# Performance work log

Measured on AMD Instinct MI355X. Metric: run time of the kernel, lower is better.

The kernel has to match this reference:

```python
import jax, jax.numpy as jnp
import numpy as np

K = 9  # kernel_size (knn neighbors, loop=True -> self included)

def setup_inputs() -> dict:
    key = jax.random.key(0)
    k1, k2, k3 = jax.random.split(key, 3)
    B, C, H, W = 8, 64, 32, 32
    OUT = 64
    x = jax.random.normal(k1, (B, C, H, W), dtype=jnp.float32)
    # SAGEConv params: lin_l (neighbor aggregate, with bias), lin_r (root, no bias)
    s = 1.0 / np.sqrt(C)
    W_l = jax.random.uniform(k2, (OUT, C), minval=-s, maxval=s, dtype=jnp.float32)
    b_l = jnp.zeros((OUT,), dtype=jnp.float32)
    W_r = jax.random.uniform(k3, (OUT, C), minval=-s, maxval=s, dtype=jnp.float32)
    return {"x": x, "W_l": W_l, "b_l": b_l, "W_r": W_r}

def _knn_mean(x_f, batches):
    # squared-euclidean pairwise distances [N, N], masked across batches
    sq = jnp.sum(x_f * x_f, axis=-1)
    dist = sq[:, None] + sq[None, :] - 2.0 * (x_f @ x_f.T)
    cross = batches[:, None] != batches[None, :]
    dist = jnp.where(cross, jnp.inf, dist)
    neg, idx = jax.lax.top_k(-dist, K)          # k nearest (self included, dist 0)
    valid = (neg != -jnp.inf).astype(x_f.dtype)  # handle degenerate last-batch node
    nbr = x_f[idx] * valid[..., None]            # [N, K, C]
    return nbr.sum(axis=1) / valid.sum(axis=1, keepdims=True)

def reference(x, W_l, b_l, W_r):
    B, C, H, Wd = x.shape
    N = B * H * Wd
    x_f = x.transpose(0, 2, 3, 1).reshape(N, C)  # flat_nodes: [B*H*W, C]
    # torch.linspace(0, B, steps=N).to(int64): truncation of i*B/(N-1)
    batches = jnp.linspace(0.0, float(B), N).astype(jnp.int32)
    mean_nbr = _knn_mean(x_f, batches)
    # SAGEConv: lin_l(mean_j x_j) + lin_r(x_i)
    return mean_nbr @ W_l.T + b_l + x_f @ W_r.T
```

## Files before the change

### kernel.cpp

```cpp
#include <hip/hip_runtime.h>
#include <cstdint>
#include <cstddef>


__global__ __launch_bounds__(256, 2) void k_dist(const float* __restrict__ x,
                                                 float* __restrict__ xf,
                                                 float* __restrict__ D) {
  __shared__ float4 As4[32 * 33];
  __shared__ float4 Bs4[32 * 33];
  __shared__ float sqA[128];
  __shared__ float sqB[128];
  int cx = blockIdx.x;
  int i0 = (int)blockIdx.y << 7;
  int s = (i0 >= 7168) ? 7168 : (i0 & ~1023);
  int j0 = s + (cx << 7);
  const float* xA = x + (((size_t)(i0 >> 10)) << 16) + (i0 & 1023);
  const float* xB = x + (((size_t)(j0 >> 10)) << 16) + (j0 & 1023);
  int t = threadIdx.x;
  int tx = t & 15, ty = t >> 4;

  float acc[8][8];
#pragma unroll
  for (int r = 0; r < 8; ++r)
#pragma unroll
    for (int c = 0; c < 8; ++c) acc[r][c] = 0.f;

#pragma unroll 1
  for (int pass = 0; pass < 2; ++pass) {
    if (pass) __syncthreads();
    int c0 = pass << 5;
#pragma unroll
    for (int i = 0; i < 4; ++i) {
      int u = t + (i << 8);
      int c = u >> 5, m4 = u & 31;
      As4[c * 33 + m4] = *(const float4*)&xA[((size_t)(c0 + c) << 10) + (m4 << 2)];
      Bs4[c * 33 + m4] = *(const float4*)&xB[((size_t)(c0 + c) << 10) + (m4 << 2)];
    }
    __syncthreads();
    {
      int m = t & 127;
      const float* base = (t < 128) ? (const float*)As4 : (const float*)Bs4;
      float p = 0.f;
#pragma unroll
      for (int c = 0; c < 32; ++c) {
        float v = base[(c * 33 + (m >> 2)) * 4 + (m & 3)];
        p = fmaf(v, v, p);
      }
      float* dst = (t < 128) ? sqA : sqB;
      if (pass == 0) dst[m] = p; else dst[m] += p;
    }
    if (cx == 0) {
#pragma unroll
      for (int i = 0; i < 16; ++i) {
        int u = t + (i << 8);
        int c = u & 31, m = u >> 5;
        xf[((size_t)(i0 + m) << 6) + c0 + c] =
            ((const float*)As4)[(c * 33 + (m >> 2)) * 4 + (m & 3)];
      }
    }
#pragma unroll 4
    for (int k = 0; k < 32; ++k) {
      float4 a0 = As4[k * 33 + ty];
      float4 a1 = As4[k * 33 + 16 + ty];
      float4 b0 = Bs4[k * 33 + tx];
      float4 b1 = Bs4[k * 33 + 16 + tx];
      float av[8] = {a0.x, a0.y, a0.z, a0.w, a1.x, a1.y, a1.z, a1.w};
      float bv[8] = {b0.x, b0.y, b0.z, b0.w, b1.x, b1.y, b1.z, b1.w};
#pragma unroll
      for (int r = 0; r < 8; ++r)
#pragma unroll
        for (int c = 0; c < 8; ++c)
          acc[r][c] = fmaf(av[r], bv[c], acc[r][c]);
    }
  }
  __syncthreads();

  int rloc[8], cloc[8];
#pragma unroll
  for (int r = 0; r < 4; ++r) { rloc[r] = (ty << 2) + r; rloc[4 + r] = 64 + (ty << 2) + r; }
#pragma unroll
  for (int c = 0; c < 4; ++c) { cloc[c] = (tx << 2) + c; cloc[4 + c] = 64 + (tx << 2) + c; }
  float sqi[8], sqj[8];
#pragma unroll
  for (int r = 0; r < 8; ++r) sqi[r] = sqA[rloc[r]];
#pragma unroll
  for (int c = 0; c < 8; ++c) sqj[c] = sqB[cloc[c]];
#pragma unroll
  for (int r = 0; r < 8; ++r) {
    size_t rb = ((size_t)(i0 + rloc[r]) << 10) + (cx << 7);
    float4 o0, o1;
    o0.x = sqi[r] + sqj[0] - 2.f * acc[r][0];
    o0.y = sqi[r] + sqj[1] - 2.f * acc[r][1];
    o0.z = sqi[r] + sqj[2] - 2.f * acc[r][2];
    o0.w = sqi[r] + sqj[3] - 2.f * acc[r][3];
    o1.x = sqi[r] + sqj[4] - 2.f * acc[r][4];
    o1.y = sqi[r] + sqj[5] - 2.f * acc[r][5];
    o1.z = sqi[r] + sqj[6] - 2.f * acc[r][6];
    o1.w = sqi[r] + sqj[7] - 2.f * acc[r][7];
    *(float4*)&D[rb + (tx << 2)] = o0;
    *(float4*)&D[rb + 64 + (tx << 2)] = o1;
  }
}

__global__ __launch_bounds__(256, 2) void k_selout(const float* __restrict__ D,
                                                   const float* __restrict__ xf,
                                                   const float* __restrict__ Wl,
                                                   const float* __restrict__ bl,
                                                   const float* __restrict__ Wr,
                                                   float* __restrict__ out) {
  __shared__ float WsL[64][65];
  __shared__ float WsR[64][65];
  int t = threadIdx.x;
#pragma unroll
  for (int i = 0; i < 16; ++i) {
    int lin = t + (i << 8);
    WsL[lin >> 6][lin & 63] = Wl[lin];
    WsR[lin >> 6][lin & 63] = Wr[lin];
  }
  __syncthreads();
  int lane = t & 63;
  float wl[64], wr[64];
#pragma unroll
  for (int c = 0; c < 64; ++c) { wl[c] = WsL[lane][c]; wr[c] = WsR[lane][c]; }
  float bias = bl[lane];
  int w = t >> 6;
  int n0 = ((int)blockIdx.x << 4) + (w << 2);

  unsigned j9[4][9];
#pragma unroll
  for (int r = 0; r < 4; ++r) {
    int n = n0 + r;
    if (n == 8191) { j9[r][0] = 8191u; continue; }
    int s = (n >= 7168) ? 7168 : (n & ~1023);
    bool mlast = (n >= 7168);
    const float* drow = D + ((size_t)n << 10);
    unsigned long long cand[16];
#pragma unroll
    for (int q = 0; q < 4; ++q) {
      float4 v = *(const float4*)&drow[(lane << 4) + (q << 2)];
      float vv[4] = {v.x, v.y, v.z, v.w};
#pragma unroll
      for (int e = 0; e < 4; ++e) {
        int slot = (q << 2) + e;
        unsigned u = __float_as_uint(vv[e]);
        u = (u & 0x80000000u) ? ~u : (u | 0x80000000u);
        cand[slot] = ((unsigned long long)u << 32) | (unsigned)((lane << 4) + slot);
      }
    }
    if (mlast && lane == 63) cand[15] = ~0ull;
    unsigned long long m1 = cand[0], m2 = cand[1];
    if (m2 < m1) { unsigned long long tt = m1; m1 = m2; m2 = tt; }
#pragma unroll
    for (int q = 2; q < 16; ++q) {
      unsigned long long c = cand[q];
      unsigned long long lo = (c < m1) ? c : m1;
      unsigned long long hi = (c < m1) ? m1 : c;
      m2 = (hi < m2) ? hi : m2;
      m1 = lo;
    }
    unsigned long long lm = m1;
    unsigned rmask = 0;
    bool stale = false;
#pragma unroll
    for (int kk = 0; kk < 9; ++kk) {
      unsigned long long g = lm;
#pragma unroll
      for (int off = 32; off; off >>= 1) {
        unsigned ghi = __shfl_xor((unsigned)(g >> 32), off, 64);
        unsigned glo = __shfl_xor((unsigned)g, off, 64);
        unsigned long long o = ((unsigned long long)ghi << 32) | glo;
        g = (o < g) ? o : g;
      }
      j9[r][kk] = (unsigned)s + ((unsigned)g & 1023u);
      if (lm == g) {
        rmask |= 1u << (unsigned)(g & 15u);
        if (!stale) { lm = m2; stale = true; }
        else {
          unsigned long long best = ~0ull;
#pragma unroll
          for (int q = 0; q < 16; ++q) {
            bool alive = ((rmask >> q) & 1u) == 0u;
            unsigned long long c = cand[q];
            best = (alive && c < best) ? c : best;
          }
          lm = best;
        }
      }
    }
  }

  float ms[4], xr[4];
#pragma unroll
  for (int r = 0; r < 4; ++r) {
    int n = n0 + r;
    int cnt = (n == 8191) ? 1 : 9;
    float msum = 0.f;
    for (int k = 0; k < cnt; ++k)
      msum += xf[((size_t)j9[r][k] << 6) + lane];
    ms[r] = msum / (float)cnt;
    xr[r] = xf[((size_t)n << 6) + lane];
  }
  float accL[4] = {0.f, 0.f, 0.f, 0.f};
  float accR[4] = {0.f, 0.f, 0.f, 0.f};
#pragma unroll
  for (int c = 0; c < 64; ++c) {
#pragma unroll
    for (int r = 0; r < 4; ++r) {
      float mc = __int_as_float(__builtin_amdgcn_readlane(__float_as_int(ms[r]), c));
      float xc = __int_as_float(__builtin_amdgcn_readlane(__float_as_int(xr[r]), c));
      accL[r] = fmaf(mc, wl[c], accL[r]);
      accR[r] = fmaf(xc, wr[c], accR[r]);
    }
  }
#pragma unroll
  for (int r = 0; r < 4; ++r)
    out[((size_t)(n0 + r) << 6) + lane] = accL[r] + accR[r] + bias;
}

extern "C" void kernel_launch(void* const* d_in, const int* in_sizes, int n_in,
                              void* d_out, int out_size, void* d_ws, size_t ws_size,
                              hipStream_t stream) {
  const float* x  = (const float*)d_in[0];
  const float* Wl = (const float*)d_in[1];
  const float* bl = (const float*)d_in[2];
  const float* Wr = (const float*)d_in[3];
  float* out = (float*)d_out;

  char* ws = (char*)d_ws;
  float* xf = (float*)(ws);
  float* D  = (float*)(ws + 2097152);

  k_dist<<<dim3(8, 64), 256, 0, stream>>>(x, xf, D);
  k_selout<<<512, 256, 0, stream>>>(D, xf, Wl, bl, Wr, out);
}
```

Measured before the change: 106.5 us.

## Apply linear layers before neighbor gather and fold projection into distance kernel

Because the mean commutes with the linear map, x·W_l^T and x·W_r^T (plus bias) are now computed once per node as extra GEMM tiles inside the distance kernel, using 64 extra blocks that reuse the tiled FMA path. The selection kernel then averages nine projected rows instead of running a per-row 64x64 matvec held in registers, which frees registers and lets it use one wave per node with higher occupancy. The load of distance candidates is also reordered so each wave reads contiguously (lane-strided float4). The xf transpose buffer is dropped; the cost is extra workspace for the yl/yr buffers and a small rounding difference from reordering the sum.

```diff
diff --git a/kernel.cpp b/kernel.cpp
--- a/kernel.cpp
+++ b/kernel.cpp
@@ -4,18 +4,28 @@
 
 
 __global__ __launch_bounds__(256, 2) void k_dist(const float* __restrict__ x,
-                                                 float* __restrict__ xf,
+                                                 const float* __restrict__ Wl,
+                                                 const float* __restrict__ Wr,
+                                                 const float* __restrict__ bl,
+                                                 float* __restrict__ yl,
+                                                 float* __restrict__ yr,
                                                  float* __restrict__ D) {
   __shared__ float4 As4[32 * 33];
   __shared__ float4 Bs4[32 * 33];
   __shared__ float sqA[128];
   __shared__ float sqB[128];
-  int cx = blockIdx.x;
-  int i0 = (int)blockIdx.y << 7;
-  int s = (i0 >= 7168) ? 7168 : (i0 & ~1023);
-  int j0 = s + (cx << 7);
+  int bx = blockIdx.x, by = blockIdx.y;
+  bool is_w = (by >= 64);
+  int i0, j0 = 0;
+  if (is_w) {
+    i0 = (((by - 64) << 3) + bx) << 7;
+  } else {
+    i0 = by << 7;
+    int s = (i0 >= 7168) ? 7168 : (i0 & ~1023);
+    j0 = s + (bx << 7);
+  }
   const float* xA = x + (((size_t)(i0 >> 10)) << 16) + (i0 & 1023);
-  const float* xB = x + (((size_t)(j0 >> 10)) << 16) + (j0 & 1023);
+  const float* xB = is_w ? xA : x + (((size_t)(j0 >> 10)) << 16) + (j0 & 1023);
   int t = threadIdx.x;
   int tx = t & 15, ty = t >> 4;
 
@@ -34,10 +44,26 @@
       int u = t + (i << 8);
       int c = u >> 5, m4 = u & 31;
       As4[c * 33 + m4] = *(const float4*)&xA[((size_t)(c0 + c) << 10) + (m4 << 2)];
-      Bs4[c * 33 + m4] = *(const float4*)&xB[((size_t)(c0 + c) << 10) + (m4 << 2)];
+    }
+    if (!is_w) {
+#pragma unroll
+      for (int i = 0; i < 4; ++i) {
+        int u = t + (i << 8);
+        int c = u >> 5, m4 = u & 31;
+        Bs4[c * 33 + m4] = *(const float4*)&xB[((size_t)(c0 + c) << 10) + (m4 << 2)];
+      }
+    } else {
+#pragma unroll
+      for (int i = 0; i < 16; ++i) {
+        int u = t + (i << 8);
+        int j = u >> 5, c = u & 31;
+        const float* Wsrc = (j < 64) ? Wl : Wr;
+        int jr = j & 63;
+        ((float*)&Bs4[c * 33 + (j >> 2)])[j & 3] = Wsrc[(jr << 6) + c0 + c];
+      }
     }
     __syncthreads();
-    {
+    if (!is_w) {
       int m = t & 127;
       const float* base = (t < 128) ? (const float*)As4 : (const float*)Bs4;
       float p = 0.f;
@@ -48,15 +74,6 @@
       }
       float* dst = (t < 128) ? sqA : sqB;
       if (pass == 0) dst[m] = p; else dst[m] += p;
-    }
-    if (cx == 0) {
-#pragma unroll
-      for (int i = 0; i < 16; ++i) {
-        int u = t + (i << 8);
-        int c = u & 31, m = u >> 5;
-        xf[((size_t)(i0 + m) << 6) + c0 + c] =
-            ((const float*)As4)[(c * 33 + (m >> 2)) * 4 + (m & 3)];
-      }
     }
 #pragma unroll 4
     for (int k = 0; k < 32; ++k) {
@@ -75,9 +92,26 @@
   }
   __syncthreads();
 
-  int rloc[8], cloc[8];
+  int rloc[8];
 #pragma unroll
   for (int r = 0; r < 4; ++r) { rloc[r] = (ty << 2) + r; rloc[4 + r] = 64 + (ty << 2) + r; }
+
+  if (is_w) {
+    float4 blv = *(const float4*)&bl[tx << 2];
+#pragma unroll
+    for (int r = 0; r < 8; ++r) {
+      int n = i0 + rloc[r];
+      float4 o0, o1;
+      o0.x = acc[r][0]; o0.y = acc[r][1]; o0.z = acc[r][2]; o0.w = acc[r][3];
+      o1.x = acc[r][4] + blv.x; o1.y = acc[r][5] + blv.y;
+      o1.z = acc[r][6] + blv.z; o1.w = acc[r][7] + blv.w;
+      *(float4*)&yl[((size_t)n << 6) + (tx << 2)] = o0;
+      *(float4*)&yr[((size_t)n << 6) + (tx << 2)] = o1;
+    }
+    return;
+  }
+
+  int cloc[8];
 #pragma unroll
   for (int c = 0; c < 4; ++c) { cloc[c] = (tx << 2) + c; cloc[4 + c] = 64 + (tx << 2) + c; }
   float sqi[8], sqj[8];
@@ -87,7 +121,7 @@
   for (int c = 0; c < 8; ++c) sqj[c] = sqB[cloc[c]];
 #pragma unroll
   for (int r = 0; r < 8; ++r) {
-    size_t rb = ((size_t)(i0 + rloc[r]) << 10) + (cx << 7);
+    size_t rb = ((size_t)(i0 + rloc[r]) << 10) + (bx << 7);
     float4 o0, o1;
     o0.x = sqi[r] + sqj[0] - 2.f * acc[r][0];
     o0.y = sqi[r] + sqj[1] - 2.f * acc[r][1];
@@ -102,49 +136,34 @@
   }
 }
 
-__global__ __launch_bounds__(256, 2) void k_selout(const float* __restrict__ D,
-                                                   const float* __restrict__ xf,
-                                                   const float* __restrict__ Wl,
-                                                   const float* __restrict__ bl,
-                                                   const float* __restrict__ Wr,
+__global__ __launch_bounds__(256, 4) void k_selout(const float* __restrict__ D,
+                                                   const float* __restrict__ yl,
+                                                   const float* __restrict__ yr,
                                                    float* __restrict__ out) {
-  __shared__ float WsL[64][65];
-  __shared__ float WsR[64][65];
   int t = threadIdx.x;
-#pragma unroll
-  for (int i = 0; i < 16; ++i) {
-    int lin = t + (i << 8);
-    WsL[lin >> 6][lin & 63] = Wl[lin];
-    WsR[lin >> 6][lin & 63] = Wr[lin];
-  }
-  __syncthreads();
   int lane = t & 63;
-  float wl[64], wr[64];
-#pragma unroll
-  for (int c = 0; c < 64; ++c) { wl[c] = WsL[lane][c]; wr[c] = WsR[lane][c]; }
-  float bias = bl[lane];
   int w = t >> 6;
-  int n0 = ((int)blockIdx.x << 4) + (w << 2);
-
-  unsigned j9[4][9];
-#pragma unroll
-  for (int r = 0; r < 4; ++r) {
-    int n = n0 + r;
-    if (n == 8191) { j9[r][0] = 8191u; continue; }
+  int n = ((int)blockIdx.x << 2) + w;
+
+  float rv = yr[((size_t)n << 6) + lane];
+  float acc;
+  if (n == 8191) {
+    acc = yl[((size_t)n << 6) + lane];
+  } else {
     int s = (n >= 7168) ? 7168 : (n & ~1023);
     bool mlast = (n >= 7168);
     const float* drow = D + ((size_t)n << 10);
     unsigned long long cand[16];
 #pragma unroll
     for (int q = 0; q < 4; ++q) {
-      float4 v = *(const float4*)&drow[(lane << 4) + (q << 2)];
+      float4 v = *(const float4*)&drow[(q << 8) + (lane << 2)];
       float vv[4] = {v.x, v.y, v.z, v.w};
 #pragma unroll
       for (int e = 0; e < 4; ++e) {
-        int slot = (q << 2) + e;
         unsigned u = __float_as_uint(vv[e]);
         u = (u & 0x80000000u) ? ~u : (u | 0x80000000u);
-        cand[slot] = ((unsigned long long)u << 32) | (unsigned)((lane << 4) + slot);
+        unsigned jj = (unsigned)((q << 8) + (lane << 2) + e);
+        cand[(q << 2) + e] = ((unsigned long long)u << 32) | jj;
       }
     }
     if (mlast && lane == 63) cand[15] = ~0ull;
@@ -161,6 +180,7 @@
     unsigned long long lm = m1;
     unsigned rmask = 0;
     bool stale = false;
+    unsigned j9[9];
 #pragma unroll
     for (int kk = 0; kk < 9; ++kk) {
       unsigned long long g = lm;
@@ -171,9 +191,10 @@
         unsigned long long o = ((unsigned long long)ghi << 32) | glo;
         g = (o < g) ? o : g;
       }
-      j9[r][kk] = (unsigned)s + ((unsigned)g & 1023u);
+      j9[kk] = (unsigned)s + ((unsigned)g & 1023u);
       if (lm == g) {
-        rmask |= 1u << (unsigned)(g & 15u);
+        unsigned slot = (((unsigned)g >> 6) & 12u) | ((unsigned)g & 3u);
+        rmask |= 1u << slot;
         if (!stale) { lm = m2; stale = true; }
         else {
           unsigned long long best = ~0ull;
@@ -187,34 +208,18 @@
         }
       }
     }
-  }
-
-  float ms[4], xr[4];
-#pragma unroll
-  for (int r = 0; r < 4; ++r) {
-    int n = n0 + r;
-    int cnt = (n == 8191) ? 1 : 9;
-    float msum = 0.f;
-    for (int k = 0; k < cnt; ++k)
-      msum += xf[((size_t)j9[r][k] << 6) + lane];
-    ms[r] = msum / (float)cnt;
-    xr[r] = xf[((size_t)n << 6) + lane];
-  }
-  float accL[4] = {0.f, 0.f, 0.f, 0.f};
-  float accR[4] = {0.f, 0.f, 0.f, 0.f};
-#pragma unroll
-  for (int c = 0; c < 64; ++c) {
-#pragma unroll
-    for (int r = 0; r < 4; ++r) {
-      float mc = __int_as_float(__builtin_amdgcn_readlane(__float_as_int(ms[r]), c));
-      float xc = __int_as_float(__builtin_amdgcn_readlane(__float_as_int(xr[r]), c));
-      accL[r] = fmaf(mc, wl[c], accL[r]);
-      accR[r] = fmaf(xc, wr[c], accR[r]);
-    }
-  }
-#pragma unroll
-  for (int r = 0; r < 4; ++r)
-    out[((size_t)(n0 + r) << 6) + lane] = accL[r] + accR[r] + bias;
+    float g0 = yl[((size_t)j9[0] << 6) + lane];
+    float g1 = yl[((size_t)j9[1] << 6) + lane];
+    float g2 = yl[((size_t)j9[2] << 6) + lane];
+    float g3 = yl[((size_t)j9[3] << 6) + lane];
+    float g4 = yl[((size_t)j9[4] << 6) + lane];
+    float g5 = yl[((size_t)j9[5] << 6) + lane];
+    float g6 = yl[((size_t)j9[6] << 6) + lane];
+    float g7 = yl[((size_t)j9[7] << 6) + lane];
+    float g8 = yl[((size_t)j9[8] << 6) + lane];
+    acc = (((g0 + g1) + (g2 + g3)) + ((g4 + g5) + (g6 + g7)) + g8) * (1.f / 9.f);
+  }
+  out[((size_t)n << 6) + lane] = acc + rv;
 }
 
 extern "C" void kernel_launch(void* const* d_in, const int* in_sizes, int n_in,
@@ -227,9 +232,10 @@
   float* out = (float*)d_out;
 
   char* ws = (char*)d_ws;
-  float* xf = (float*)(ws);
-  float* D  = (float*)(ws + 2097152);
-
-  k_dist<<<dim3(8, 64), 256, 0, stream>>>(x, xf, D);
-  k_selout<<<512, 256, 0, stream>>>(D, xf, Wl, bl, Wr, out);
+  float* yl = (float*)(ws);
+  float* yr = (float*)(ws + 2097152);
+  float* D  = (float*)(ws + 4194304);
+
+  k_dist<<<dim3(8, 72), 256, 0, stream>>>(x, Wl, Wr, bl, yl, yr, D);
+  k_selout<<<2048, 256, 0, stream>>>(D, yl, yr, out);
 }
```

After: 113.0 us. +6.2%, slower.

## Fuse distance, top-k selection and SAGE projection into one kernel via LDS

Applied to the files above, without the earlier changes.

Merges the distance kernel and the selection/output kernel into a single kernel. Each block computes a 16x1024 distance strip for its rows directly into shared memory, so the 8192x1024 distance matrix is never written to or read back from global memory. Neighbours are gathered straight from the original NCHW input, and the weights are staged in LDS instead of registers. In exchange, each block reloads its batch's full 1024-node feature slab and recomputes squared norms redundantly. It also uses about 72KB of LDS per block, which may limit occupancy.

```diff
diff --git a/kernel.cpp b/kernel.cpp
--- a/kernel.cpp
+++ b/kernel.cpp
@@ -3,67 +3,65 @@
 #include <cstddef>
 
 
-__global__ __launch_bounds__(256, 2) void k_dist(const float* __restrict__ x,
-                                                 float* __restrict__ xf,
-                                                 float* __restrict__ D) {
-  __shared__ float4 As4[32 * 33];
-  __shared__ float4 Bs4[32 * 33];
-  __shared__ float sqA[128];
-  __shared__ float sqB[128];
-  int cx = blockIdx.x;
-  int i0 = (int)blockIdx.y << 7;
-  int s = (i0 >= 7168) ? 7168 : (i0 & ~1023);
-  int j0 = s + (cx << 7);
-  const float* xA = x + (((size_t)(i0 >> 10)) << 16) + (i0 & 1023);
-  const float* xB = x + (((size_t)(j0 >> 10)) << 16) + (j0 & 1023);
-  int t = threadIdx.x;
-  int tx = t & 15, ty = t >> 4;
+typedef float nf4 __attribute__((ext_vector_type(4)));
+
+__global__ __launch_bounds__(256, 2) void k_all(const float* __restrict__ x,
+                                                const float* __restrict__ Wl,
+                                                const float* __restrict__ bl,
+                                                const float* __restrict__ Wr,
+                                                float* __restrict__ out) {
+  __shared__ float R0[16384];
+  __shared__ float Asf[1024];
+  __shared__ float sqX[1024];
+  float4* Xs4 = (float4*)R0;
+  float4* As4 = (float4*)Asf;
+  float4* sqX4 = (float4*)sqX;
+
+  int bi = (int)blockIdx.x, t = threadIdx.x;
+  int n0 = bi << 4;
+  int s = (n0 >= 7168) ? 7168 : (n0 & ~1023);
+  const float* xb = x + (((size_t)(s >> 10)) << 16);
+  const float* xrow = x + (((size_t)(n0 >> 10)) << 16) + (n0 & 1023);
+
+  {
+    int c = t >> 2, r4 = t & 3;
+    As4[(c << 2) + r4] = *(const float4*)&xrow[((size_t)c << 10) + (r4 << 2)];
+  }
 
   float acc[8][8];
 #pragma unroll
   for (int r = 0; r < 8; ++r)
 #pragma unroll
     for (int c = 0; c < 8; ++c) acc[r][c] = 0.f;
+  float4 p4 = {0.f, 0.f, 0.f, 0.f};
+  int h = t >> 7, cg = t & 127;
 
 #pragma unroll 1
-  for (int pass = 0; pass < 2; ++pass) {
-    if (pass) __syncthreads();
-    int c0 = pass << 5;
-#pragma unroll
-    for (int i = 0; i < 4; ++i) {
-      int u = t + (i << 8);
-      int c = u >> 5, m4 = u & 31;
-      As4[c * 33 + m4] = *(const float4*)&xA[((size_t)(c0 + c) << 10) + (m4 << 2)];
-      Bs4[c * 33 + m4] = *(const float4*)&xB[((size_t)(c0 + c) << 10) + (m4 << 2)];
+  for (int ks = 0; ks < 4; ++ks) {
+    if (ks) __syncthreads();
+    int k0 = ks << 4;
+#pragma unroll 4
+    for (int i = 0; i < 16; ++i) {
+      int lin = t + (i << 8);
+      int kc = lin >> 8, j4 = lin & 255;
+      Xs4[(kc << 8) + j4] =
+          *(const float4*)&xb[((size_t)(k0 + kc) << 10) + (j4 << 2)];
     }
     __syncthreads();
-    {
-      int m = t & 127;
-      const float* base = (t < 128) ? (const float*)As4 : (const float*)Bs4;
-      float p = 0.f;
-#pragma unroll
-      for (int c = 0; c < 32; ++c) {
-        float v = base[(c * 33 + (m >> 2)) * 4 + (m & 3)];
-        p = fmaf(v, v, p);
-      }
-      float* dst = (t < 128) ? sqA : sqB;
-      if (pass == 0) dst[m] = p; else dst[m] += p;
-    }
-    if (cx == 0) {
-#pragma unroll
-      for (int i = 0; i < 16; ++i) {
-        int u = t + (i << 8);
-        int c = u & 31, m = u >> 5;
-        xf[((size_t)(i0 + m) << 6) + c0 + c] =
-            ((const float*)As4)[(c * 33 + (m >> 2)) * 4 + (m & 3)];
-      }
-    }
-#pragma unroll 4
-    for (int k = 0; k < 32; ++k) {
-      float4 a0 = As4[k * 33 + ty];
-      float4 a1 = As4[k * 33 + 16 + ty];
-      float4 b0 = Bs4[k * 33 + tx];
-      float4 b1 = Bs4[k * 33 + 16 + tx];
+#pragma unroll
+    for (int kc = 0; kc < 16; ++kc) {
+      float4 v = Xs4[(kc << 8) + t];
+      p4.x = fmaf(v.x, v.x, p4.x);
+      p4.y = fmaf(v.y, v.y, p4.y);
+      p4.z = fmaf(v.z, v.z, p4.z);
+      p4.w = fmaf(v.w, v.w, p4.w);
+    }
+#pragma unroll
+    for (int kc = 0; kc < 16; ++kc) {
+      float4 a0 = As4[((k0 + kc) << 2) + (h << 1)];
+      float4 a1 = As4[((k0 + kc) << 2) + (h << 1) + 1];
+      float4 b0 = Xs4[(kc << 8) + cg];
+      float4 b1 = Xs4[(kc << 8) + 128 + cg];
       float av[8] = {a0.x, a0.y, a0.z, a0.w, a1.x, a1.y, a1.z, a1.w};
       float bv[8] = {b0.x, b0.y, b0.z, b0.w, b1.x, b1.y, b1.z, b1.w};
 #pragma unroll
@@ -73,78 +71,50 @@
           acc[r][c] = fmaf(av[r], bv[c], acc[r][c]);
     }
   }
-  __syncthreads();
-
-  int rloc[8], cloc[8];
-#pragma unroll
-  for (int r = 0; r < 4; ++r) { rloc[r] = (ty << 2) + r; rloc[4 + r] = 64 + (ty << 2) + r; }
-#pragma unroll
-  for (int c = 0; c < 4; ++c) { cloc[c] = (tx << 2) + c; cloc[4 + c] = 64 + (tx << 2) + c; }
-  float sqi[8], sqj[8];
-#pragma unroll
-  for (int r = 0; r < 8; ++r) sqi[r] = sqA[rloc[r]];
-#pragma unroll
-  for (int c = 0; c < 8; ++c) sqj[c] = sqB[cloc[c]];
-#pragma unroll
-  for (int r = 0; r < 8; ++r) {
-    size_t rb = ((size_t)(i0 + rloc[r]) << 10) + (cx << 7);
-    float4 o0, o1;
-    o0.x = sqi[r] + sqj[0] - 2.f * acc[r][0];
-    o0.y = sqi[r] + sqj[1] - 2.f * acc[r][1];
-    o0.z = sqi[r] + sqj[2] - 2.f * acc[r][2];
-    o0.w = sqi[r] + sqj[3] - 2.f * acc[r][3];
-    o1.x = sqi[r] + sqj[4] - 2.f * acc[r][4];
-    o1.y = sqi[r] + sqj[5] - 2.f * acc[r][5];
-    o1.z = sqi[r] + sqj[6] - 2.f * acc[r][6];
-    o1.w = sqi[r] + sqj[7] - 2.f * acc[r][7];
-    *(float4*)&D[rb + (tx << 2)] = o0;
-    *(float4*)&D[rb + 64 + (tx << 2)] = o1;
-  }
-}
-
-__global__ __launch_bounds__(256, 2) void k_selout(const float* __restrict__ D,
-                                                   const float* __restrict__ xf,
-                                                   const float* __restrict__ Wl,
-                                                   const float* __restrict__ bl,
-                                                   const float* __restrict__ Wr,
-                                                   float* __restrict__ out) {
-  __shared__ float WsL[64][65];
-  __shared__ float WsR[64][65];
-  int t = threadIdx.x;
-#pragma unroll
-  for (int i = 0; i < 16; ++i) {
-    int lin = t + (i << 8);
-    WsL[lin >> 6][lin & 63] = Wl[lin];
-    WsR[lin >> 6][lin & 63] = Wr[lin];
-  }
-  __syncthreads();
-  int lane = t & 63;
-  float wl[64], wr[64];
-#pragma unroll
-  for (int c = 0; c < 64; ++c) { wl[c] = WsL[lane][c]; wr[c] = WsR[lane][c]; }
-  float bias = bl[lane];
-  int w = t >> 6;
-  int n0 = ((int)blockIdx.x << 4) + (w << 2);
-
-  unsigned j9[4][9];
-#pragma unroll
-  for (int r = 0; r < 4; ++r) {
-    int n = n0 + r;
-    if (n == 8191) { j9[r][0] = 8191u; continue; }
-    int s = (n >= 7168) ? 7168 : (n & ~1023);
+  sqX4[t] = p4;
+  __syncthreads();
+
+  {
+    float4 sj0 = sqX4[cg];
+    float4 sj1 = sqX4[128 + cg];
+    int jb = (n0 - s) + (h << 3);
+#pragma unroll
+    for (int r = 0; r < 8; ++r) {
+      float si = sqX[jb + r];
+      nf4 o0 = {si + sj0.x - 2.f * acc[r][0], si + sj0.y - 2.f * acc[r][1],
+                si + sj0.z - 2.f * acc[r][2], si + sj0.w - 2.f * acc[r][3]};
+      nf4 o1 = {si + sj1.x - 2.f * acc[r][4], si + sj1.y - 2.f * acc[r][5],
+                si + sj1.z - 2.f * acc[r][6], si + sj1.w - 2.f * acc[r][7]};
+      int row = (h << 3) + r;
+      *(nf4*)&R0[(row << 10) + (cg << 2)] = o0;
+      *(nf4*)&R0[(row << 10) + 512 + (cg << 2)] = o1;
+    }
+  }
+  __syncthreads();
+
+  int lane = t & 63, w = t >> 6;
+  float msum[4], xr[4];
+  int cnt[4];
+#pragma unroll 1
+  for (int rr = 0; rr < 4; ++rr) {
+    int rl = (w << 2) + rr;
+    int n = n0 + rl;
+    float xself = x[(((size_t)(n >> 10)) << 16) + ((size_t)lane << 10) + (n & 1023)];
+    xr[rr] = xself;
+    if (n == 8191) { msum[rr] = xself; cnt[rr] = 1; continue; }
+    cnt[rr] = 9;
     bool mlast = (n >= 7168);
-    const float* drow = D + ((size_t)n << 10);
     unsigned long long cand[16];
 #pragma unroll
     for (int q = 0; q < 4; ++q) {
-      float4 v = *(const float4*)&drow[(lane << 4) + (q << 2)];
+      nf4 v = *(const nf4*)&R0[(rl << 10) + (q << 8) + (lane << 2)];
       float vv[4] = {v.x, v.y, v.z, v.w};
 #pragma unroll
       for (int e = 0; e < 4; ++e) {
-        int slot = (q << 2) + e;
         unsigned u = __float_as_uint(vv[e]);
         u = (u & 0x80000000u) ? ~u : (u | 0x80000000u);
-        cand[slot] = ((unsigned long long)u << 32) | (unsigned)((lane << 4) + slot);
+        unsigned jj = (unsigned)((q << 8) + (lane << 2) + e);
+        cand[(q << 2) + e] = ((unsigned long long)u << 32) | jj;
       }
     }
     if (mlast && lane == 63) cand[15] = ~0ull;
@@ -161,6 +131,7 @@
     unsigned long long lm = m1;
     unsigned rmask = 0;
     bool stale = false;
+    unsigned jloc[9];
 #pragma unroll
     for (int kk = 0; kk < 9; ++kk) {
       unsigned long long g = lm;
@@ -171,9 +142,10 @@
         unsigned long long o = ((unsigned long long)ghi << 32) | glo;
         g = (o < g) ? o : g;
       }
-      j9[r][kk] = (unsigned)s + ((unsigned)g & 1023u);
+      jloc[kk] = (unsigned)g & 1023u;
       if (lm == g) {
-        rmask |= 1u << (unsigned)(g & 15u);
+        unsigned slot = (((unsigned)g >> 6) & 12u) | ((unsigned)g & 3u);
+        rmask |= 1u << slot;
         if (!stale) { lm = m2; stale = true; }
         else {
           unsigned long long best = ~0ull;
@@ -187,34 +159,46 @@
         }
       }
     }
-  }
-
-  float ms[4], xr[4];
-#pragma unroll
-  for (int r = 0; r < 4; ++r) {
-    int n = n0 + r;
-    int cnt = (n == 8191) ? 1 : 9;
-    float msum = 0.f;
-    for (int k = 0; k < cnt; ++k)
-      msum += xf[((size_t)j9[r][k] << 6) + lane];
-    ms[r] = msum / (float)cnt;
-    xr[r] = xf[((size_t)n << 6) + lane];
-  }
+    const float* gx = xb + ((size_t)lane << 10);
+    float g0 = gx[jloc[0]], g1 = gx[jloc[1]], g2 = gx[jloc[2]];
+    float g3 = gx[jloc[3]], g4 = gx[jloc[4]], g5 = gx[jloc[5]];
+    float g6 = gx[jloc[6]], g7 = gx[jloc[7]], g8 = gx[jloc[8]];
+    msum[rr] = (((g0 + g1) + (g2 + g3)) + ((g4 + g5) + (g6 + g7))) + g8;
+  }
+  __syncthreads();
+
+#pragma unroll 4
+  for (int i = 0; i < 16; ++i) {
+    int lin = t + (i << 8);
+    int o = lin >> 6, c = lin & 63;
+    R0[o * 65 + c] = Wl[lin];
+    R0[4160 + o * 65 + c] = Wr[lin];
+  }
+  __syncthreads();
+
+  float bias = bl[lane];
+  float ms[4];
+#pragma unroll
+  for (int rr = 0; rr < 4; ++rr)
+    ms[rr] = (cnt[rr] == 9) ? msum[rr] * (1.f / 9.f) : msum[rr];
   float accL[4] = {0.f, 0.f, 0.f, 0.f};
   float accR[4] = {0.f, 0.f, 0.f, 0.f};
 #pragma unroll
   for (int c = 0; c < 64; ++c) {
-#pragma unroll
-    for (int r = 0; r < 4; ++r) {
-      float mc = __int_as_float(__builtin_amdgcn_readlane(__float_as_int(ms[r]), c));
-      float xc = __int_as_float(__builtin_amdgcn_readlane(__float_as_int(xr[r]), c));
-      accL[r] = fmaf(mc, wl[c], accL[r]);
-      accR[r] = fmaf(xc, wr[c], accR[r]);
-    }
-  }
-#pragma unroll
-  for (int r = 0; r < 4; ++r)
-    out[((size_t)(n0 + r) << 6) + lane] = accL[r] + accR[r] + bias;
+    float wlc = R0[lane * 65 + c];
+    float wrc = R0[4160 + lane * 65 + c];
+#pragma unroll
+    for (int rr = 0; rr < 4; ++rr) {
+      float mc = __int_as_float(__builtin_amdgcn_readlane(__float_as_int(ms[rr]), c));
+      float xc = __int_as_float(__builtin_amdgcn_readlane(__float_as_int(xr[rr]), c));
+      accL[rr] = fmaf(mc, wlc, accL[rr]);
+      accR[rr] = fmaf(xc, wrc, accR[rr]);
+    }
+  }
+#pragma unroll
+  for (int rr = 0; rr < 4; ++rr)
+    __builtin_nontemporal_store(accL[rr] + accR[rr] + bias,
+                                &out[((size_t)(n0 + (w << 2) + rr) << 6) + lane]);
 }
 
 extern "C" void kernel_launch(void* const* d_in, const int* in_sizes, int n_in,
@@ -225,11 +209,7 @@
   const float* bl = (const float*)d_in[2];
   const float* Wr = (const float*)d_in[3];
   float* out = (float*)d_out;
-
-  char* ws = (char*)d_ws;
-  float* xf = (float*)(ws);
-  float* D  = (float*)(ws + 2097152);
-
-  k_dist<<<dim3(8, 64), 256, 0, stream>>>(x, xf, D);
-  k_selout<<<512, 256, 0, stream>>>(D, xf, Wl, bl, Wr, out);
+  (void)d_ws; (void)ws_size;
+
+  k_all<<<dim3(512), 256, 0, stream>>>(x, Wl, bl, Wr, out);
 }
```

After: 104.6 us. Within noise of the previous version (-1.8%).
